# Kernel tuning notes

Measured on AMD Instinct MI355X. Metric: run time of the kernel, lower is better.

Reference implementation:

```python
import jax, jax.numpy as jnp
import numpy as np

WS = 32  # window size hardcoded in the original module

def _dwconv7(x, w, b):
    # x: (B,C,H,W), w: (C,1,7,7) depthwise
    y = jax.lax.conv_general_dilated(
        x, w, window_strides=(1, 1), padding='SAME',
        dimension_numbers=('NCHW', 'OIHW', 'NCHW'),
        feature_group_count=x.shape[1])
    return y + b[None, :, None, None]


def setup_inputs() -> dict:
    key = jax.random.key(0)
    ks = jax.random.split(key, 9)
    B, C, H, W = 4, 64, 128, 128
    x = jax.random.normal(ks[0], (B, C, H, W), dtype=jnp.float32)
    s = 0.05
    conv1_w = jax.random.normal(ks[1], (C, 1, 7, 7), dtype=jnp.float32) * s
    conv1_b = jax.random.normal(ks[2], (C,), dtype=jnp.float32) * s
    conv2_w = jax.random.normal(ks[3], (C, C), dtype=jnp.float32) * s
    conv2_b = jax.random.normal(ks[4], (C,), dtype=jnp.float32) * s
    conv3_w = jax.random.normal(ks[5], (C, C), dtype=jnp.float32) * s
    conv3_b = jax.random.normal(ks[6], (C,), dtype=jnp.float32) * s
    conv4_w = jax.random.normal(ks[7], (C, C), dtype=jnp.float32) * s
    conv4_b = jax.random.normal(ks[8], (C,), dtype=jnp.float32) * s
    return {'x': x, 'conv1_w': conv1_w, 'conv1_b': conv1_b,
            'conv2_w': conv2_w, 'conv2_b': conv2_b,
            'conv3_w': conv3_w, 'conv3_b': conv3_b,
            'conv4_w': conv4_w, 'conv4_b': conv4_b}


def reference(x, conv1_w, conv1_b, conv2_w, conv2_b, conv3_w, conv3_b, conv4_w, conv4_b):
    B, C, H, W = x.shape
    scale = jnp.asarray(C, x.dtype) ** -0.5
    h = _dwconv7(x, conv1_w, conv1_b)
    # window partition: (B,C,H,W) -> (N, C, WS*WS) with N = B*(H/WS)*(W/WS)
    hw = h.reshape(B, C, H // WS, WS, W // WS, WS)
    hw = hw.transpose(0, 2, 4, 1, 3, 5).reshape(-1, C, WS * WS)  # (N,C,P)
    # 1x1 convs as channel matmuls
    q = jnp.einsum('oc,ncp->nop', conv2_w, hw) + conv2_b[None, :, None]  # (N,C,P)
    k = jnp.einsum('oc,ncp->nop', conv3_w, hw) + conv3_b[None, :, None]  # (N,C,P)
    # att = k^T @ q * scale, softmax over dim 1 (first spatial axis)
    att = jnp.einsum('ncp,ncq->npq', k, q) * scale  # (N,P,P)
    att = jax.nn.softmax(att, axis=1)
    out = jnp.einsum('ncp,npq->ncq', hw, att)  # (N,C,P)
    out = jnp.einsum('oc,ncq->noq', conv4_w, out) + conv4_b[None, :, None]
    # un-partition back to (B,C,H,W)
    out = out.reshape(B, H // WS, W // WS, C, WS, WS)
    out = out.transpose(0, 3, 1, 4, 2, 5).reshape(B, C, H, W)
    return out
```

## Files before the change

### kernel.cpp

```cpp
#include <hip/hip_runtime.h>

typedef unsigned int  u32;
typedef unsigned short u16;
typedef short s16x8 __attribute__((ext_vector_type(8)));
typedef float f32x16 __attribute__((ext_vector_type(16)));

#define BB   4
#define CC   64
#define HH   128
#define WW   128
#define NWIN 64
#define PP   1024

__device__ __forceinline__ u16 f2bf(float f) {
  u32 x = __float_as_uint(f);
  return (u16)((x + 0x7fffu + ((x >> 16) & 1u)) >> 16);
}
__device__ __forceinline__ u32 pk2(float a, float b) {
  return (u32)f2bf(a) | ((u32)f2bf(b) << 16);
}

__global__ __launch_bounds__(256)
void dwconv_kernel(const float* __restrict__ x, const float* __restrict__ w,
                   const float* __restrict__ bias, float* __restrict__ hw,
                   u16* __restrict__ vb, float* __restrict__ vsum) {
  int blk = blockIdx.x;
  int n = blk >> 6, c = blk & 63;
  int b = n >> 4, wy = (n >> 2) & 3, wx = n & 3;
  int y0 = wy * 32 - 3, x0 = wx * 32 - 3;
  __shared__ float patch[38][40];
  __shared__ float wf[49];
  __shared__ float wsum[4];
  int tid = threadIdx.x;
  if (tid < 49) wf[tid] = w[c * 49 + tid];
  const float* xp = x + (size_t)(b * CC + c) * HH * WW;
  for (int i = tid; i < 38 * 38; i += 256) {
    int py = i / 38, px = i - py * 38;
    int gy = y0 + py, gx = x0 + px;
    float v = 0.f;
    if (gy >= 0 && gy < HH && gx >= 0 && gx < WW) v = xp[gy * WW + gx];
    patch[py][px] = v;
  }
  __syncthreads();
  float bv = bias[c];
  int ox = tid & 31, oy0 = (tid >> 5) * 4;
  float* outp = hw + (size_t)(n * CC + c) * PP;
  u16* vbp = vb + (size_t)(n * CC + c) * PP;
  float psum = 0.f;
  for (int rr = 0; rr < 4; ++rr) {
    int oy = oy0 + rr;
    float acc = bv;
    #pragma unroll
    for (int dy = 0; dy < 7; ++dy)
      #pragma unroll
      for (int dx = 0; dx < 7; ++dx)
        acc = fmaf(patch[oy + dy][ox + dx], wf[dy * 7 + dx], acc);
    outp[oy * 32 + ox] = acc;
    vbp[oy * 32 + ox] = f2bf(acc);
    psum += acc;
  }
  #pragma unroll
  for (int off = 1; off < 64; off <<= 1) psum += __shfl_xor(psum, off);
  if ((tid & 63) == 0) wsum[tid >> 6] = psum;
  __syncthreads();
  if (tid == 0) vsum[blk] = (wsum[0] + wsum[1]) + (wsum[2] + wsum[3]);
}

__global__ __launch_bounds__(256)
void qk_kernel(const float* __restrict__ hw,
               const float* __restrict__ w2, const float* __restrict__ b2,
               const float* __restrict__ w3, const float* __restrict__ b3,
               u16* __restrict__ qT, u16* __restrict__ kT) {
  int n = blockIdx.x >> 4;
  int chunk = blockIdx.x & 15;
  int tid = threadIdx.x;
  int lane = tid & 63, wvi = tid >> 6;
  int l31 = lane & 31, hi = lane >> 5;
  int phalf = wvi & 1, ochalf = wvi >> 1;
  int p0 = (chunk << 6) + (phalf << 5);
  int oc0 = ochalf << 5;

  union FU { u32 u[4]; s16x8 v; };

  s16x8 bq[4], bk[4];
  {
    const float* w2r = w2 + (oc0 + l31) * 64 + (hi << 3);
    const float* w3r = w3 + (oc0 + l31) * 64 + (hi << 3);
    #pragma unroll
    for (int kst = 0; kst < 4; ++kst) {
      float4 a = *(const float4*)(w2r + kst * 16);
      float4 b = *(const float4*)(w2r + kst * 16 + 4);
      FU f;
      f.u[0] = pk2(a.x * 0.125f, a.y * 0.125f);
      f.u[1] = pk2(a.z * 0.125f, a.w * 0.125f);
      f.u[2] = pk2(b.x * 0.125f, b.y * 0.125f);
      f.u[3] = pk2(b.z * 0.125f, b.w * 0.125f);
      bq[kst] = f.v;
      float4 c = *(const float4*)(w3r + kst * 16);
      float4 d = *(const float4*)(w3r + kst * 16 + 4);
      f.u[0] = pk2(c.x, c.y); f.u[1] = pk2(c.z, c.w);
      f.u[2] = pk2(d.x, d.y); f.u[3] = pk2(d.z, d.w);
      bk[kst] = f.v;
    }
  }

  f32x16 accq, acck;
  #pragma unroll
  for (int j = 0; j < 16; ++j) { accq[j] = 0.f; acck[j] = 0.f; }

  const float* hbase = hw + ((size_t)n << 16) + (size_t)(hi << 3) * PP
                       + p0 + l31;
  #pragma unroll
  for (int kst = 0; kst < 4; ++kst) {
    const float* hp = hbase + (size_t)(kst * 16) * PP;
    float h[8];
    #pragma unroll
    for (int e = 0; e < 8; ++e) h[e] = hp[e * PP];
    FU fh, fl;
    #pragma unroll
    for (int t = 0; t < 4; ++t) {
      u32 ph;
      asm("v_cvt_pk_bf16_f32 %0, %1, %2"
          : "=v"(ph) : "v"(h[2 * t]), "v"(h[2 * t + 1]));
      fh.u[t] = ph;
      float r0 = h[2 * t]     - __uint_as_float(ph << 16);
      float r1 = h[2 * t + 1] - __uint_as_float(ph & 0xffff0000u);
      u32 pl;
      asm("v_cvt_pk_bf16_f32 %0, %1, %2" : "=v"(pl) : "v"(r0), "v"(r1));
      fl.u[t] = pl;
    }
    accq = __builtin_amdgcn_mfma_f32_32x32x16_bf16(fh.v, bq[kst], accq, 0, 0, 0);
    accq = __builtin_amdgcn_mfma_f32_32x32x16_bf16(fl.v, bq[kst], accq, 0, 0, 0);
    acck = __builtin_amdgcn_mfma_f32_32x32x16_bf16(fh.v, bk[kst], acck, 0, 0, 0);
    acck = __builtin_amdgcn_mfma_f32_32x32x16_bf16(fl.v, bk[kst], acck, 0, 0, 0);
  }

  float biasq = b2[oc0 + l31] * 0.125f;
  float biask = b3[oc0 + l31];
  u16* qrow = qT + (((size_t)n << 10) + p0) * 64 + oc0 + l31;
  u16* krow = kT + (((size_t)n << 10) + p0) * 64 + oc0 + l31;
  #pragma unroll
  for (int r = 0; r < 16; ++r) {
    int pr = (r & 3) + ((r >> 2) << 3) + (hi << 2);
    qrow[pr * 64] = f2bf(accq[r] + biasq);
    krow[pr * 64] = f2bf(acck[r] + biask);
  }
}

__global__ __launch_bounds__(256)
void attn_kernel(const u16* __restrict__ qT, const u16* __restrict__ kT,
                 const u16* __restrict__ vB, const float* __restrict__ vsum,
                 float* __restrict__ ob) {
  int bid = blockIdx.x;
  int w = (bid & 7) * 64 + (bid >> 3);
  int n = w >> 3, qb = w & 7;
  int tid = threadIdx.x;

  __shared__ __align__(16) unsigned char QsB[16384];
  __shared__ __align__(16) unsigned char KsB[8192];
  __shared__ __align__(16) unsigned char VsB[8192];
  __shared__ float l_inv[4][32];

  const size_t nbase = (size_t)n << 16;

  {
    const u16* qg = qT + nbase + ((size_t)qb << 13);
    for (int i = tid; i < 1024; i += 256) {
      int row = i >> 3, c8 = i & 7;
      uint4 v = *(const uint4*)(qg + row * 64 + c8 * 8);
      *(uint4*)(QsB + row * 128 + ((c8 * 16) ^ ((row & 7) << 4))) = v;
    }
  }

  int lane = tid & 63, wv = tid >> 6;
  int l31 = lane & 31, hi = lane >> 5;
  int sz = (lane & 7) << 4;
  int hi16 = hi << 4;

  f32x16 o0, o1;
  #pragma unroll
  for (int j = 0; j < 16; ++j) { o0[j] = 0.f; o1[j] = 0.f; }
  float lsum = 0.f;

  const u16* kg = kT + nbase;
  const u16* vg = vB + nbase;
  int qrow = (wv << 5) + l31;

  for (int pt = 0; pt < 16; ++pt) {
    __syncthreads();
    int p0 = pt << 6;
    for (int i = tid; i < 512; i += 256) {
      int row = i >> 3, c8 = i & 7;
      int dst = row * 128 + ((c8 * 16) ^ ((row & 7) << 4));
      uint4 kv4 = *(const uint4*)(kg + (size_t)(p0 + row) * 64 + c8 * 8);
      *(uint4*)(KsB + dst) = kv4;
      uint4 vv4 = *(const uint4*)(vg + (size_t)row * 1024 + p0 + c8 * 8);
      *(uint4*)(VsB + dst) = vv4;
    }
    __syncthreads();

    f32x16 s0, s1;
    #pragma unroll
    for (int j = 0; j < 16; ++j) { s0[j] = 0.f; s1[j] = 0.f; }
    #pragma unroll
    for (int kc = 0; kc < 4; ++kc) {
      int cb = kc * 32 + hi16;
      s16x8 b  = *(const s16x8*)(QsB + qrow * 128 + (cb ^ sz));
      s16x8 a0 = *(const s16x8*)(KsB + l31 * 128 + (cb ^ sz));
      s16x8 a1 = *(const s16x8*)(KsB + (32 + l31) * 128 + (cb ^ sz));
      s0 = __builtin_amdgcn_mfma_f32_32x32x16_bf16(a0, b, s0, 0, 0, 0);
      s1 = __builtin_amdgcn_mfma_f32_32x32x16_bf16(a1, b, s1, 0, 0, 0);
    }

    #pragma unroll
    for (int j = 0; j < 16; ++j) {
      float e = __expf(s0[j]); lsum += e; s0[j] = e - 1.0f;
    }
    #pragma unroll
    for (int j = 0; j < 16; ++j) {
      float e = __expf(s1[j]); lsum += e; s1[j] = e - 1.0f;
    }

    u32 t0,t1,t2,t3,t4,t5,t6,t7, u0,u1,u2,u3,u4,u5,u6,u7;
#define CVT(d, a, b) asm("v_cvt_pk_bf16_f32 %0, %1, %2" : "=v"(d) : "v"(a), "v"(b))
#define SWP(a, b)    asm("v_permlane32_swap_b32 %0, %1" : "+v"(a), "+v"(b))
    CVT(t0, s0[0],  s0[1]);  CVT(t1, s0[2],  s0[3]);
    CVT(t2, s0[4],  s0[5]);  CVT(t3, s0[6],  s0[7]);
    CVT(t4, s0[8],  s0[9]);  CVT(t5, s0[10], s0[11]);
    CVT(t6, s0[12], s0[13]); CVT(t7, s0[14], s0[15]);
    SWP(t0, t2); SWP(t1, t3); SWP(t4, t6); SWP(t5, t7);
    CVT(u0, s1[0],  s1[1]);  CVT(u1, s1[2],  s1[3]);
    CVT(u2, s1[4],  s1[5]);  CVT(u3, s1[6],  s1[7]);
    CVT(u4, s1[8],  s1[9]);  CVT(u5, s1[10], s1[11]);
    CVT(u6, s1[12], s1[13]); CVT(u7, s1[14], s1[15]);
    SWP(u0, u2); SWP(u1, u3); SWP(u4, u6); SWP(u5, u7);
#undef CVT
#undef SWP
    union FU { u32 u[4]; s16x8 v; };
    FU fA; fA.u[0]=t0; fA.u[1]=t1; fA.u[2]=t2; fA.u[3]=t3;
    FU fB; fB.u[0]=t4; fB.u[1]=t5; fB.u[2]=t6; fB.u[3]=t7;
    FU fC; fC.u[0]=u0; fC.u[1]=u1; fC.u[2]=u2; fC.u[3]=u3;
    FU fD; fD.u[0]=u4; fD.u[1]=u5; fD.u[2]=u6; fD.u[3]=u7;

#define PV_STEP(frag, pb) do { \
      s16x8 bv0 = *(const s16x8*)(VsB + l31 * 128 + ((pb) ^ sz)); \
      s16x8 bv1 = *(const s16x8*)(VsB + (32 + l31) * 128 + ((pb) ^ sz)); \
      o0 = __builtin_amdgcn_mfma_f32_32x32x16_bf16(frag, bv0, o0, 0, 0, 0); \
      o1 = __builtin_amdgcn_mfma_f32_32x32x16_bf16(frag, bv1, o1, 0, 0, 0); \
    } while (0)
    PV_STEP(fA.v, 0 + hi16);
    PV_STEP(fB.v, 32 + hi16);
    PV_STEP(fC.v, 64 + hi16);
    PV_STEP(fD.v, 96 + hi16);
#undef PV_STEP
  }

  lsum += __shfl_xor(lsum, 32);
  if (hi == 0) l_inv[wv][l31] = 1.0f / lsum;

  float vs0 = vsum[(n << 6) + l31];
  float vs1 = vsum[(n << 6) + 32 + l31];
  #pragma unroll
  for (int r = 0; r < 16; ++r) {
    int qr = (r & 3) + ((r >> 2) << 3) + (hi << 2);
    float li = l_inv[wv][qr];
    size_t base = nbase + ((size_t)((qb << 7) + (wv << 5) + qr) << 6);
    ob[base + l31]      = (vs0 + o0[r]) * li;
    ob[base + 32 + l31] = (vs1 + o1[r]) * li;
  }
}

__global__ __launch_bounds__(256)
void conv4_kernel(const float* __restrict__ ob,
                  const float* __restrict__ w4, const float* __restrict__ b4,
                  float* __restrict__ outp) {
  int n = blockIdx.x >> 4;
  int chunk = blockIdx.x & 15;
  int tid = threadIdx.x;
  int lane = tid & 63, wvi = tid >> 6;
  int l31 = lane & 31, hi = lane >> 5;
  int qhalf = wvi & 1, ochalf = wvi >> 1;
  int q0 = (chunk << 6) + (qhalf << 5);
  int oc0 = ochalf << 5;

  union FU { u32 u[4]; s16x8 v; };

  s16x8 aw[4];
  {
    const float* w4r = w4 + (oc0 + l31) * 64 + (hi << 3);
    #pragma unroll
    for (int kst = 0; kst < 4; ++kst) {
      float4 a = *(const float4*)(w4r + kst * 16);
      float4 b = *(const float4*)(w4r + kst * 16 + 4);
      FU f;
      f.u[0] = pk2(a.x, a.y); f.u[1] = pk2(a.z, a.w);
      f.u[2] = pk2(b.x, b.y); f.u[3] = pk2(b.z, b.w);
      aw[kst] = f.v;
    }
  }

  f32x16 acc;
  #pragma unroll
  for (int j = 0; j < 16; ++j) acc[j] = 0.f;
  const float* obr = ob + (((size_t)n << 10) + q0 + l31) * 64 + (hi << 3);
  #pragma unroll
  for (int kst = 0; kst < 4; ++kst) {
    float4 a = *(const float4*)(obr + kst * 16);
    float4 b = *(const float4*)(obr + kst * 16 + 4);
    FU f;
    f.u[0] = pk2(a.x, a.y); f.u[1] = pk2(a.z, a.w);
    f.u[2] = pk2(b.x, b.y); f.u[3] = pk2(b.z, b.w);
    acc = __builtin_amdgcn_mfma_f32_32x32x16_bf16(aw[kst], f.v, acc, 0, 0, 0);
  }

  int b_ = n >> 4, wy = (n >> 2) & 3, wx = n & 3;
  int y = wy * 32 + (q0 >> 5);
  int x = wx * 32 + l31;
  #pragma unroll
  for (int r = 0; r < 16; ++r) {
    int oc = oc0 + (r & 3) + ((r >> 2) << 3) + (hi << 2);
    outp[((size_t)(b_ * CC + oc) * HH + y) * WW + x] = acc[r] + b4[oc];
  }
}

extern "C" void kernel_launch(void* const* d_in, const int* in_sizes, int n_in,
                              void* d_out, int out_size, void* d_ws, size_t ws_size,
                              hipStream_t stream) {
  const float* x  = (const float*)d_in[0];
  const float* w1 = (const float*)d_in[1];
  const float* b1 = (const float*)d_in[2];
  const float* w2 = (const float*)d_in[3];
  const float* b2 = (const float*)d_in[4];
  const float* w3 = (const float*)d_in[5];
  const float* b3 = (const float*)d_in[6];
  const float* w4 = (const float*)d_in[7];
  const float* b4 = (const float*)d_in[8];
  float* outp = (float*)d_out;

  char* wsb = (char*)d_ws;
  float* hw   = (float*)wsb;
  u16*   qT   = (u16*)(wsb + (16u << 20));
  u16*   kT   = (u16*)(wsb + (24u << 20));
  u16*   vb   = (u16*)(wsb + (32u << 20));
  float* ob   = (float*)(wsb + (40u << 20));
  float* vsum = (float*)(wsb + (56u << 20));

  dwconv_kernel<<<NWIN * CC, 256, 0, stream>>>(x, w1, b1, hw, vb, vsum);
  qk_kernel   <<<NWIN * 16, 256, 0, stream>>>(hw, w2, b2, w3, b3, qT, kT);
  attn_kernel <<<NWIN * 8,  256, 0, stream>>>(qT, kT, vb, vsum, ob);
  conv4_kernel<<<NWIN * 16, 256, 0, stream>>>(ob, w4, b4, outp);
}
```

Baseline: 165.3 us.

## Fuse conv4 projection into attention epilogue and register-block depthwise conv

The attention kernel now writes its normalized output as bf16 into reused shared memory, then applies the conv4 1x1 projection with MFMA and writes the final NCHW output directly. This removes the fp32 intermediate buffer round trip and one kernel launch. Separately, the depthwise conv computes four adjacent outputs per thread from vectorized shared-memory row loads, with float4 and packed bf16 stores. The fused epilogue adds register pressure and reuses the Q shared buffer, so it relies on every wave having finished reading Q before any wave overwrites it.

Measured after the change: 151.5 us. 8.3% less time.

```diff
diff --git a/kernel.cpp b/kernel.cpp
--- a/kernel.cpp
+++ b/kernel.cpp
@@ -43,22 +43,30 @@
   }
   __syncthreads();
   float bv = bias[c];
-  int ox = tid & 31, oy0 = (tid >> 5) * 4;
-  float* outp = hw + (size_t)(n * CC + c) * PP;
-  u16* vbp = vb + (size_t)(n * CC + c) * PP;
-  float psum = 0.f;
-  for (int rr = 0; rr < 4; ++rr) {
-    int oy = oy0 + rr;
-    float acc = bv;
-    #pragma unroll
-    for (int dy = 0; dy < 7; ++dy)
-      #pragma unroll
-      for (int dx = 0; dx < 7; ++dx)
-        acc = fmaf(patch[oy + dy][ox + dx], wf[dy * 7 + dx], acc);
-    outp[oy * 32 + ox] = acc;
-    vbp[oy * 32 + ox] = f2bf(acc);
-    psum += acc;
-  }
+  int yy = tid >> 3;
+  int xg = (tid & 7) << 2;
+  float o0_ = bv, o1_ = bv, o2_ = bv, o3_ = bv;
+  #pragma unroll
+  for (int dy = 0; dy < 7; ++dy) {
+    const float* pr = &patch[yy + dy][xg];
+    float4 ra = *(const float4*)pr;
+    float4 rb = *(const float4*)(pr + 4);
+    float4 rc = *(const float4*)(pr + 8);
+    float rv[12] = {ra.x, ra.y, ra.z, ra.w, rb.x, rb.y, rb.z, rb.w,
+                    rc.x, rc.y, rc.z, rc.w};
+    #pragma unroll
+    for (int dx = 0; dx < 7; ++dx) {
+      float wgt = wf[dy * 7 + dx];
+      o0_ = fmaf(rv[dx],     wgt, o0_);
+      o1_ = fmaf(rv[dx + 1], wgt, o1_);
+      o2_ = fmaf(rv[dx + 2], wgt, o2_);
+      o3_ = fmaf(rv[dx + 3], wgt, o3_);
+    }
+  }
+  size_t obase = (size_t)(n * CC + c) * PP + yy * 32 + xg;
+  *(float4*)(hw + obase) = make_float4(o0_, o1_, o2_, o3_);
+  *(uint2*)(vb + obase) = make_uint2(pk2(o0_, o1_), pk2(o2_, o3_));
+  float psum = (o0_ + o1_) + (o2_ + o3_);
   #pragma unroll
   for (int off = 1; off < 64; off <<= 1) psum += __shfl_xor(psum, off);
   if ((tid & 63) == 0) wsum[tid >> 6] = psum;
@@ -150,7 +158,8 @@
 __global__ __launch_bounds__(256)
 void attn_kernel(const u16* __restrict__ qT, const u16* __restrict__ kT,
                  const u16* __restrict__ vB, const float* __restrict__ vsum,
-                 float* __restrict__ ob) {
+                 const float* __restrict__ w4, const float* __restrict__ b4,
+                 float* __restrict__ outp) {
   int bid = blockIdx.x;
   int w = (bid & 7) * 64 + (bid >> 3);
   int n = w >> 3, qb = w & 7;
@@ -260,66 +269,61 @@
 
   float vs0 = vsum[(n << 6) + l31];
   float vs1 = vsum[(n << 6) + 32 + l31];
+  int g0 = l31 >> 3, g1 = (32 + l31) >> 3;
+  int bi = (l31 & 7) << 1;
   #pragma unroll
   for (int r = 0; r < 16; ++r) {
     int qr = (r & 3) + ((r >> 2) << 3) + (hi << 2);
+    int row = (wv << 5) + qr;
     float li = l_inv[wv][qr];
-    size_t base = nbase + ((size_t)((qb << 7) + (wv << 5) + qr) << 6);
-    ob[base + l31]      = (vs0 + o0[r]) * li;
-    ob[base + 32 + l31] = (vs1 + o1[r]) * li;
-  }
-}
-
-__global__ __launch_bounds__(256)
-void conv4_kernel(const float* __restrict__ ob,
-                  const float* __restrict__ w4, const float* __restrict__ b4,
-                  float* __restrict__ outp) {
-  int n = blockIdx.x >> 4;
-  int chunk = blockIdx.x & 15;
-  int tid = threadIdx.x;
-  int lane = tid & 63, wvi = tid >> 6;
-  int l31 = lane & 31, hi = lane >> 5;
-  int qhalf = wvi & 1, ochalf = wvi >> 1;
-  int q0 = (chunk << 6) + (qhalf << 5);
-  int oc0 = ochalf << 5;
-
-  union FU { u32 u[4]; s16x8 v; };
-
-  s16x8 aw[4];
+    int rs = (row & 7) << 4;
+    *(u16*)(QsB + row * 128 + ((g0 << 4) ^ rs) + bi) = f2bf((vs0 + o0[r]) * li);
+    *(u16*)(QsB + row * 128 + ((g1 << 4) ^ rs) + bi) = f2bf((vs1 + o1[r]) * li);
+  }
+
+  union FU2 { u32 u[4]; s16x8 v; };
+  int orow = (wv << 5) + l31;
+  int osw = (orow & 7) << 4;
+  s16x8 bf[4];
+  #pragma unroll
+  for (int kst = 0; kst < 4; ++kst)
+    bf[kst] = *(const s16x8*)(QsB + orow * 128 + ((((kst << 1) + hi) << 4) ^ osw));
+
+  f32x16 d2a, d2b;
+  #pragma unroll
+  for (int j = 0; j < 16; ++j) { d2a[j] = 0.f; d2b[j] = 0.f; }
   {
-    const float* w4r = w4 + (oc0 + l31) * 64 + (hi << 3);
+    const float* w4r = w4 + l31 * 64 + (hi << 3);
     #pragma unroll
     for (int kst = 0; kst < 4; ++kst) {
       float4 a = *(const float4*)(w4r + kst * 16);
       float4 b = *(const float4*)(w4r + kst * 16 + 4);
-      FU f;
+      FU2 f;
       f.u[0] = pk2(a.x, a.y); f.u[1] = pk2(a.z, a.w);
       f.u[2] = pk2(b.x, b.y); f.u[3] = pk2(b.z, b.w);
-      aw[kst] = f.v;
-    }
-  }
-
-  f32x16 acc;
-  #pragma unroll
-  for (int j = 0; j < 16; ++j) acc[j] = 0.f;
-  const float* obr = ob + (((size_t)n << 10) + q0 + l31) * 64 + (hi << 3);
-  #pragma unroll
-  for (int kst = 0; kst < 4; ++kst) {
-    float4 a = *(const float4*)(obr + kst * 16);
-    float4 b = *(const float4*)(obr + kst * 16 + 4);
-    FU f;
-    f.u[0] = pk2(a.x, a.y); f.u[1] = pk2(a.z, a.w);
-    f.u[2] = pk2(b.x, b.y); f.u[3] = pk2(b.z, b.w);
-    acc = __builtin_amdgcn_mfma_f32_32x32x16_bf16(aw[kst], f.v, acc, 0, 0, 0);
+      d2a = __builtin_amdgcn_mfma_f32_32x32x16_bf16(f.v, bf[kst], d2a, 0, 0, 0);
+    }
+    const float* w4r2 = w4 + (32 + l31) * 64 + (hi << 3);
+    #pragma unroll
+    for (int kst = 0; kst < 4; ++kst) {
+      float4 a = *(const float4*)(w4r2 + kst * 16);
+      float4 b = *(const float4*)(w4r2 + kst * 16 + 4);
+      FU2 f;
+      f.u[0] = pk2(a.x, a.y); f.u[1] = pk2(a.z, a.w);
+      f.u[2] = pk2(b.x, b.y); f.u[3] = pk2(b.z, b.w);
+      d2b = __builtin_amdgcn_mfma_f32_32x32x16_bf16(f.v, bf[kst], d2b, 0, 0, 0);
+    }
   }
 
   int b_ = n >> 4, wy = (n >> 2) & 3, wx = n & 3;
-  int y = wy * 32 + (q0 >> 5);
+  int y = wy * 32 + (qb << 2) + wv;
   int x = wx * 32 + l31;
+  float* obase = outp + ((size_t)b_ * CC * HH + y) * WW + x;
   #pragma unroll
   for (int r = 0; r < 16; ++r) {
-    int oc = oc0 + (r & 3) + ((r >> 2) << 3) + (hi << 2);
-    outp[((size_t)(b_ * CC + oc) * HH + y) * WW + x] = acc[r] + b4[oc];
+    int ocr = (r & 3) + ((r >> 2) << 3) + (hi << 2);
+    obase[(size_t)ocr * HH * WW]        = d2a[r] + b4[ocr];
+    obase[(size_t)(32 + ocr) * HH * WW] = d2b[r] + b4[32 + ocr];
   }
 }
 
@@ -342,11 +346,9 @@
   u16*   qT   = (u16*)(wsb + (16u << 20));
   u16*   kT   = (u16*)(wsb + (24u << 20));
   u16*   vb   = (u16*)(wsb + (32u << 20));
-  float* ob   = (float*)(wsb + (40u << 20));
-  float* vsum = (float*)(wsb + (56u << 20));
+  float* vsum = (float*)(wsb + (40u << 20));
 
   dwconv_kernel<<<NWIN * CC, 256, 0, stream>>>(x, w1, b1, hw, vb, vsum);
   qk_kernel   <<<NWIN * 16, 256, 0, stream>>>(hw, w2, b2, w3, b3, qT, kT);
-  attn_kernel <<<NWIN * 8,  256, 0, stream>>>(qT, kT, vb, vsum, ob);
-  conv4_kernel<<<NWIN * 16, 256, 0, stream>>>(ob, w4, b4, outp);
-}
+  attn_kernel <<<NWIN * 8,  256, 0, stream>>>(qT, kT, vb, vsum, w4, b4, outp);
+}
```
